# Optimization experiments

Hardware: AMD Instinct MI355X
Metric: run time of the kernel (lower is better)

Reference implementation:

```python
import jax, jax.numpy as jnp
import numpy as np

B, S, D = 2, 2048, 2048
H, G = 32, 8            # n_head, n_kv_groups
DH = D // H             # 64
HG = H // G             # heads per group = 4


def setup_inputs() -> dict:
    key = jax.random.key(0)
    ks = jax.random.split(key, 7)
    kv_dim = G * DH
    return {
        "q": jax.random.normal(ks[0], (B, S, D), jnp.float32),
        "k": jax.random.normal(ks[1], (B, S, D), jnp.float32),
        "v": jax.random.normal(ks[2], (B, S, D), jnp.float32),
        "mask": jnp.tril(jnp.ones((S, S), jnp.bool_)),  # causal
        "w_q": jax.random.normal(ks[3], (D, D), jnp.float32) * 0.02,
        "w_k": jax.random.normal(ks[4], (kv_dim, D), jnp.float32) * 0.02,
        "w_v": jax.random.normal(ks[5], (kv_dim, D), jnp.float32) * 0.02,
        "w_out": jax.random.normal(ks[6], (D, D), jnp.float32) * 0.02,
    }


def reference(q, k, v, mask, w_q, w_k, w_v, w_out):
    scale = 1.0 / np.sqrt(DH).astype(np.float32)
    # projections (F.linear: x @ W.T)
    qp = (q @ w_q.T).reshape(B, S, G, HG, DH)   # [b s g h d]
    kp = (k @ w_k.T).reshape(B, S, G, DH)       # [b t g d]
    vp = (v @ w_v.T).reshape(B, S, G, DH)
    # grouped attention scores [b g h s t]
    scores = jnp.einsum('bsghd,btgd->bghst', qp, kp) * scale
    scores = jnp.where(mask[None, None, None], scores, jnp.float32(-jnp.inf))
    attn = jax.nn.softmax(scores, axis=-1)
    out = jnp.einsum('bghst,btgd->bsghd', attn, vp).reshape(B, S, D)
    return out @ w_out.T
```

## Files before the change

### kernel.cpp

```cpp
#include <hip/hip_runtime.h>
#include <hip/hip_bf16.h>
#include <stdint.h>

#define B_SZ 2
#define S_LEN 2048
#define D_MODEL 2048
#define NH 32
#define NG 8
#define HGRP 4
#define DHEAD 64
#define KV_DIM 512
#define M_TOK 4096
#define KVB 64
#define QBLK 256

typedef __attribute__((ext_vector_type(8))) short bf16x8;
typedef __attribute__((ext_vector_type(4))) float f32x4;
typedef __attribute__((ext_vector_type(16))) float f32x16;

__device__ inline unsigned short f2bf(float x) {
    uint32_t u = __builtin_bit_cast(uint32_t, x);
    uint32_t r = (u + 0x7fffu + ((u >> 16) & 1u)) >> 16;
    return (unsigned short)r;
}

__device__ inline uint32_t cvtpk(float lo, float hi) {
    uint32_t r;
    asm("v_cvt_pk_bf16_f32 %0, %1, %2" : "=v"(r) : "v"(lo), "v"(hi));
    return r;
}

__device__ inline void plswap(uint32_t& a, uint32_t& b) {
    asm volatile("v_permlane32_swap_b32 %0, %1" : "+v"(a), "+v"(b));
}

__device__ inline float bf2f(unsigned short u) {
    uint32_t x = ((uint32_t)u) << 16;
    return __builtin_bit_cast(float, x);
}

__device__ inline void async_copy16(const void* g, void* l) {
    __builtin_amdgcn_global_load_lds(
        (const __attribute__((address_space(1))) void*)g,
        (__attribute__((address_space(3))) void*)l,
        16, 0, 0);
}

__device__ inline void gbar() {
    asm volatile("" ::: "memory");
    __builtin_amdgcn_s_barrier();
    asm volatile("" ::: "memory");
}
__device__ inline void lgkm0() {
    asm volatile("s_waitcnt lgkmcnt(0)" ::: "memory");
    __builtin_amdgcn_sched_barrier(0);
}

__device__ inline float vmax16(const f32x16& v) {
    float a0 = fmaxf(v[0], v[1]), a1 = fmaxf(v[2], v[3]);
    float a2 = fmaxf(v[4], v[5]), a3 = fmaxf(v[6], v[7]);
    float a4 = fmaxf(v[8], v[9]), a5 = fmaxf(v[10], v[11]);
    float a6 = fmaxf(v[12], v[13]), a7 = fmaxf(v[14], v[15]);
    float b0 = fmaxf(a0, a1), b1 = fmaxf(a2, a3);
    float b2 = fmaxf(a4, a5), b3 = fmaxf(a6, a7);
    return fmaxf(fmaxf(b0, b1), fmaxf(b2, b3));
}
__device__ inline float vsum16(const f32x16& v) {
    float a0 = v[0] + v[1], a1 = v[2] + v[3], a2 = v[4] + v[5], a3 = v[6] + v[7];
    float a4 = v[8] + v[9], a5 = v[10] + v[11], a6 = v[12] + v[13], a7 = v[14] + v[15];
    float b0 = a0 + a1, b1 = a2 + a3, b2 = a4 + a5, b3 = a6 + a7;
    return (b0 + b1) + (b2 + b3);
}

__global__ __launch_bounds__(256) void cvt_w(const float* __restrict__ wq,
                                             const float* __restrict__ wk,
                                             const float* __restrict__ wv,
                                             const float* __restrict__ wo,
                                             unsigned short* __restrict__ wqb,
                                             unsigned short* __restrict__ wkvb,
                                             unsigned short* __restrict__ wob) {
    const int i = blockIdx.x * 256 + threadIdx.x;
    const float* src; unsigned short* dst; int j;
    if (i < 524288)      { src = wq; dst = wqb; j = i; }
    else if (i < 655360) { src = wk; dst = wkvb; j = i - 524288; }
    else if (i < 786432) { src = wv; dst = wkvb + (size_t)KV_DIM * D_MODEL; j = i - 655360; }
    else                 { src = wo; dst = wob; j = i - 786432; }
    const float4* p = reinterpret_cast<const float4*>(src) + (size_t)j * 2;
    float4 a = p[0], b = p[1];
    union { unsigned short u[8]; uint4 v4; } r;
    r.u[0] = f2bf(a.x); r.u[1] = f2bf(a.y); r.u[2] = f2bf(a.z); r.u[3] = f2bf(a.w);
    r.u[4] = f2bf(b.x); r.u[5] = f2bf(b.y); r.u[6] = f2bf(b.z); r.u[7] = f2bf(b.w);
    reinterpret_cast<uint4*>(dst)[j] = r.v4;
}

#define SCALE_Q 0.1803368867f
#define GK 2048

__global__ __launch_bounds__(512, 2) void gemm8p(const float* __restrict__ Aqf,
                                                 const float* __restrict__ Akf,
                                                 const float* __restrict__ Avf,
                                                 const unsigned short* __restrict__ Bq,
                                                 const unsigned short* __restrict__ Bkv,
                                                 unsigned short* __restrict__ out_q,
                                                 unsigned short* __restrict__ out_k,
                                                 unsigned short* __restrict__ out_v) {
    __shared__ __align__(16) char lds[131072];

    const int tid = threadIdx.x;
    const int lane = tid & 63;
    const int w = tid >> 6;
    const int wm = w >> 2, wn = w & 3;
    const int l15 = lane & 15, l4 = lane >> 4;

    int bid = blockIdx.x;
    bid = (bid & 7) * 24 + (bid >> 3);
    const int mb = bid & 15, nb = bid >> 4;
    const int m0 = mb * 256;

    const float* Af;
    const unsigned short* Bp;
    int mode = 0, n0q = 0;
    if (nb < 8) {
        Af = Aqf; Bp = Bq + (size_t)(nb * 256) * GK; mode = 0; n0q = nb * 256;
    } else if (nb < 10) {
        Af = Akf; Bp = Bkv + (size_t)((nb - 8) * 256) * GK; mode = 1; n0q = (nb - 8) * 256;
    } else {
        Af = Avf; Bp = Bkv + (size_t)((nb - 10) * 256 + 512) * GK; mode = 2; n0q = (nb - 10) * 256;
    }

    const int srow = tid >> 3;
    const int gcol = (((tid & 7) * 16) ^ ((srow & 7) << 4)) >> 1;
    char* const myl = lds + tid * 16;

    float4 av[8];
    auto issueA = [&](int tile) {
#pragma unroll
        for (int h = 0; h < 2; ++h)
#pragma unroll
            for (int r2 = 0; r2 < 2; ++r2) {
                const float* s = Af + (size_t)(m0 + h * 128 + srow + r2 * 64) * GK + tile * 64 + gcol;
                av[(h * 2 + r2) * 2 + 0] = *reinterpret_cast<const float4*>(s);
                av[(h * 2 + r2) * 2 + 1] = *reinterpret_cast<const float4*>(s + 4);
            }
    };
    auto writeA = [&](int tile) {
#pragma unroll
        for (int h = 0; h < 2; ++h)
#pragma unroll
            for (int r2 = 0; r2 < 2; ++r2) {
                const float4 x = av[(h * 2 + r2) * 2 + 0];
                const float4 y = av[(h * 2 + r2) * 2 + 1];
                uint4 o;
                o.x = cvtpk(x.x, x.y); o.y = cvtpk(x.z, x.w);
                o.z = cvtpk(y.x, y.y); o.w = cvtpk(y.z, y.w);
                *reinterpret_cast<uint4*>(myl + (tile & 1) * 32768 + h * 16384 + r2 * 8192) = o;
            }
    };
    auto stageB = [&](int tile, int half) {
        char* dst = myl + 65536 + (tile & 1) * 32768 + half * 16384;
        const unsigned short* src = Bp + (size_t)(half * 128 + srow) * GK + tile * 64 + gcol;
        async_copy16(src, dst);
        async_copy16(src + (size_t)64 * GK, dst + 8192);
    };

    bf16x8 af[4][2], bf[4][2];
    auto loadA = [&](int buf, int mhalf) {
        const char* base = lds + buf * 32768;
#pragma unroll
        for (int mi = 0; mi < 4; ++mi) {
            const int r = wm * 128 + mhalf * 64 + mi * 16 + l15;
#pragma unroll
            for (int ks = 0; ks < 2; ++ks)
                af[mi][ks] = *reinterpret_cast<const bf16x8*>(
                    base + r * 128 + ((ks * 64 + l4 * 16) ^ ((r & 7) << 4)));
        }
    };
    auto loadB = [&](int buf, int nhalf) {
        const char* base = lds + 65536 + buf * 32768;
#pragma unroll
        for (int ni2 = 0; ni2 < 2; ++ni2) {
            const int ni = nhalf * 2 + ni2;
            const int r = wn * 64 + ni * 16 + l15;
#pragma unroll
            for (int ks = 0; ks < 2; ++ks)
                bf[ni][ks] = *reinterpret_cast<const bf16x8*>(
                    base + r * 128 + ((ks * 64 + l4 * 16) ^ ((r & 7) << 4)));
        }
    };

    f32x4 acc[8][4] = {};
    auto mfma16 = [&](int mq, int nq) {
        __builtin_amdgcn_s_setprio(1);
#pragma unroll
        for (int mi = 0; mi < 4; ++mi)
#pragma unroll
            for (int ni2 = 0; ni2 < 2; ++ni2)
#pragma unroll
                for (int ks = 0; ks < 2; ++ks)
                    acc[mq * 4 + mi][nq * 2 + ni2] = __builtin_amdgcn_mfma_f32_16x16x32_bf16(
                        af[mi][ks], bf[nq * 2 + ni2][ks], acc[mq * 4 + mi][nq * 2 + ni2], 0, 0, 0);
        __builtin_amdgcn_s_setprio(0);
    };

    issueA(0);
    stageB(0, 0); stageB(0, 1); stageB(1, 0); stageB(1, 1);
    writeA(0);
    asm volatile("s_waitcnt vmcnt(4) lgkmcnt(0)" ::: "memory");
    gbar();

    for (int i = 0; i < 16; ++i) {
        const int u = 2 * i;
        const bool nl = (i < 15);
        loadA(0, 0); loadB(0, 0); issueA(u + 1);
        gbar(); lgkm0(); mfma16(0, 0); gbar();
        loadB(0, 1);
        gbar(); lgkm0(); mfma16(0, 1); gbar();
        loadA(0, 1); if (nl) stageB(u + 2, 0);
        gbar(); lgkm0(); mfma16(1, 0); gbar();
        if (nl) stageB(u + 2, 1);
        gbar(); mfma16(1, 1);
        if (nl) asm volatile("s_waitcnt vmcnt(4)" ::: "memory");
        else    asm volatile("s_waitcnt vmcnt(0)" ::: "memory");
        writeA(u + 1);
        asm volatile("s_waitcnt lgkmcnt(0)" ::: "memory");
        gbar();
        loadA(1, 0); loadB(1, 0); if (nl) issueA(u + 2);
        gbar(); lgkm0(); mfma16(0, 0); gbar();
        loadB(1, 1);
        gbar(); lgkm0(); mfma16(0, 1); gbar();
        loadA(1, 1); if (nl) stageB(u + 3, 0);
        gbar(); lgkm0(); mfma16(1, 0); gbar();
        if (nl) stageB(u + 3, 1);
        gbar(); mfma16(1, 1);
        if (nl) {
            asm volatile("s_waitcnt vmcnt(4)" ::: "memory");
            writeA(u + 2);
        }
        asm volatile("s_waitcnt lgkmcnt(0)" ::: "memory");
        gbar();
    }

    if (mode == 0) {
#pragma unroll
        for (int mi = 0; mi < 8; ++mi) {
            const int row = m0 + wm * 128 + mi * 16 + l4 * 4;
#pragma unroll
            for (int ni = 0; ni < 4; ++ni) {
                const int col = n0q + wn * 64 + ni * 16 + l15;
#pragma unroll
                for (int r = 0; r < 4; ++r)
                    out_q[(size_t)(row + r) * D_MODEL + col] = f2bf(acc[mi][ni][r] * SCALE_Q);
            }
        }
    } else if (mode == 1) {
#pragma unroll
        for (int mi = 0; mi < 8; ++mi) {
            const int row = m0 + wm * 128 + mi * 16 + l4 * 4;
#pragma unroll
            for (int ni = 0; ni < 4; ++ni) {
                const int col = n0q + wn * 64 + ni * 16 + l15;
#pragma unroll
                for (int r = 0; r < 4; ++r)
                    out_k[(size_t)(row + r) * KV_DIM + col] = f2bf(acc[mi][ni][r]);
            }
        }
    } else {
        const int bb = m0 >> 11;
#pragma unroll
        for (int mi = 0; mi < 8; ++mi) {
            const int tok = (m0 & 2047) + wm * 128 + mi * 16 + l4 * 4;
#pragma unroll
            for (int ni = 0; ni < 4; ++ni) {
                const int c = n0q + wn * 64 + ni * 16 + l15;
                const int g = c >> 6, dh = c & 63;
                uint2 pk;
                pk.x = cvtpk(acc[mi][ni][0], acc[mi][ni][1]);
                pk.y = cvtpk(acc[mi][ni][2], acc[mi][ni][3]);
                *reinterpret_cast<uint2*>(out_v + (size_t)((bb * NG + g) * DHEAD + dh) * S_LEN + tok) = pk;
            }
        }
    }
}

__global__ __launch_bounds__(512, 1) void gemm8o(const unsigned short* __restrict__ A,
                                                 const unsigned short* __restrict__ B,
                                                 float* __restrict__ C) {
    __shared__ __align__(16) char lds[98304];

    const int tid = threadIdx.x;
    const int lane = tid & 63;
    const int w = tid >> 6;
    const int wm = w >> 1, wn = w & 1;
    const int l15 = lane & 15, l4 = lane >> 4;

    int bid = blockIdx.x;
    bid = (bid & 7) * 32 + (bid >> 3);
    const int mb = bid & 15, nb = bid >> 4;
    const int m0 = mb * 256, n0 = nb * 128;
    const unsigned short* Bp = B + (size_t)n0 * GK;

    const int srow = tid >> 3;
    const int gcol = (((tid & 7) * 16) ^ ((srow & 7) << 4)) >> 1;

    auto stageA = [&](int tile, int half) {
        char* dst = lds + (tile & 1) * 32768 + half * 16384 + tid * 16;
        const unsigned short* src = A + (size_t)(m0 + half * 128 + srow) * GK + tile * 64 + gcol;
        async_copy16(src, dst);
        async_copy16(src + (size_t)64 * GK, dst + 8192);
    };
    auto stageB = [&](int tile, int half) {
        char* dst = lds + 65536 + (tile & 1) * 16384 + half * 8192 + tid * 16;
        const unsigned short* src = Bp + (size_t)(half * 64 + srow) * GK + tile * 64 + gcol;
        async_copy16(src, dst);
    };

    bf16x8 af[2][2], bf[4][2];
    auto loadA2 = [&](int buf, int mhalf) {
        const char* base = lds + buf * 32768;
#pragma unroll
        for (int mi = 0; mi < 2; ++mi) {
            const int r = wm * 64 + mhalf * 32 + mi * 16 + l15;
#pragma unroll
            for (int ks = 0; ks < 2; ++ks)
                af[mi][ks] = *reinterpret_cast<const bf16x8*>(
                    base + r * 128 + ((ks * 64 + l4 * 16) ^ ((r & 7) << 4)));
        }
    };
    auto loadB2 = [&](int buf, int nhalf) {
        const char* base = lds + 65536 + buf * 16384;
#pragma unroll
        for (int ni2 = 0; ni2 < 2; ++ni2) {
            const int ni = nhalf * 2 + ni2;
            const int r = wn * 64 + ni * 16 + l15;
#pragma unroll
            for (int ks = 0; ks < 2; ++ks)
                bf[ni][ks] = *reinterpret_cast<const bf16x8*>(
                    base + r * 128 + ((ks * 64 + l4 * 16) ^ ((r & 7) << 4)));
        }
    };

    f32x4 acc[4][4] = {};
    auto mfma8 = [&](int mq, int nq) {
        __builtin_amdgcn_s_setprio(1);
#pragma unroll
        for (int mi = 0; mi < 2; ++mi)
#pragma unroll
            for (int ni2 = 0; ni2 < 2; ++ni2)
#pragma unroll
                for (int ks = 0; ks < 2; ++ks)
                    acc[mq * 2 + mi][nq * 2 + ni2] = __builtin_amdgcn_mfma_f32_16x16x32_bf16(
                        af[mi][ks], bf[nq * 2 + ni2][ks], acc[mq * 2 + mi][nq * 2 + ni2], 0, 0, 0);
        __builtin_amdgcn_s_setprio(0);
    };

    stageA(0, 0); stageA(0, 1); stageB(0, 0); stageB(0, 1); stageB(1, 0); stageB(1, 1);
    asm volatile("s_waitcnt vmcnt(2)" ::: "memory");
    gbar();

    for (int i = 0; i < 16; ++i) {
        const int u = 2 * i;
        const bool nl = (i < 15);
        loadA2(0, 0); loadB2(0, 0); stageA(u + 1, 0);
        gbar(); lgkm0(); mfma8(0, 0); gbar();
        loadB2(0, 1); stageA(u + 1, 1);
        gbar(); lgkm0(); mfma8(0, 1); gbar();
        loadA2(0, 1); if (nl) stageB(u + 2, 0);
        gbar(); lgkm0(); mfma8(1, 0); gbar();
        if (nl) stageB(u + 2, 1);
        gbar(); mfma8(1, 1);
        if (nl) asm volatile("s_waitcnt vmcnt(2)" ::: "memory");
        else    asm volatile("s_waitcnt vmcnt(0)" ::: "memory");
        gbar();
        loadA2(1, 0); loadB2(1, 0); if (nl) stageA(u + 2, 0);
        gbar(); lgkm0(); mfma8(0, 0); gbar();
        loadB2(1, 1); if (nl) stageA(u + 2, 1);
        gbar(); lgkm0(); mfma8(0, 1); gbar();
        loadA2(1, 1); if (nl) stageB(u + 3, 0);
        gbar(); lgkm0(); mfma8(1, 0); gbar();
        if (nl) stageB(u + 3, 1);
        gbar(); mfma8(1, 1);
        if (nl) asm volatile("s_waitcnt vmcnt(2)" ::: "memory");
        gbar();
    }

#pragma unroll
    for (int mi = 0; mi < 4; ++mi) {
        const int row = m0 + wm * 64 + mi * 16 + l4 * 4;
#pragma unroll
        for (int ni = 0; ni < 4; ++ni) {
            const int col = n0 + wn * 64 + ni * 16 + l15;
#pragma unroll
            for (int r = 0; r < 4; ++r)
                C[(size_t)(row + r) * D_MODEL + col] = acc[mi][ni][r];
        }
    }
}

__constant__ unsigned char sl_qi[16] = {7,7,7,6,6,6,5,5,5,4,4,3,3,2,1,0};
__constant__ unsigned char sl_j0[16] = {0,11,22,0,10,19,0,8,16,0,10,0,8,0,0,0};
__constant__ unsigned char sl_j1[16] = {11,22,32,10,19,28,8,16,24,10,20,8,16,12,8,4};
__constant__ unsigned char sl_pt[16] = {0,1,2,0,1,2,0,1,2,0,1,0,1,0,0,0};
__constant__ unsigned char pb_base[5] = {0,2,4,7,10};

__global__ __launch_bounds__(512, 4) void attn6_kernel(const unsigned short* __restrict__ qp,
                                                       const unsigned short* __restrict__ kp,
                                                       const unsigned short* __restrict__ vpT,
                                                       unsigned short* __restrict__ attn_out,
                                                       unsigned short* __restrict__ partO,
                                                       float* __restrict__ ml) {
    __shared__ __align__(16) unsigned short Ks[2][KVB * 64];
    __shared__ __align__(16) unsigned short Vs[2][KVB * 64];

    const int tid = threadIdx.x;
    const int lane = tid & 63;
    const int w = tid >> 6;
    const int l31 = lane & 31, hi = lane >> 5;
    const int sr = tid >> 3, sc = tid & 7;
    const int sgcol = (((sc * 16) ^ ((sr & 7) << 4)) >> 1);
    char* const kdst0 = (char*)Ks[0] + tid * 16;
    char* const kdst1 = (char*)Ks[1] + tid * 16;
    char* const vdst0 = (char*)Vs[0] + tid * 16;
    char* const vdst1 = (char*)Vs[1] + tid * 16;

    const int item = blockIdx.x;
    const int slot = item >> 6;
    const int bh = item & 63;
    const int qi = sl_qi[slot];
    const int j0 = sl_j0[slot];
    const int j1 = sl_j1[slot];
    const int part = sl_pt[slot];
    const bool merged = (qi >= 3);
    const int b = bh >> 5, head = bh & 31, g = head >> 2;
    const int s0 = qi * QBLK;
    const int m = s0 + w * 32 + l31;
    const int mmin = s0 + w * 32;
    const int mmaxw = mmin + 31;

    bf16x8 qf[4];
    {
        const unsigned short* qrow = qp + (size_t)(b * S_LEN + m) * D_MODEL + head * DHEAD + hi * 8;
#pragma unroll
        for (int k = 0; k < 4; ++k)
            qf[k] = *reinterpret_cast<const bf16x8*>(qrow + k * 16);
    }

    const unsigned short* kbase = kp + (size_t)(b * S_LEN + sr) * KV_DIM + g * DHEAD + sgcol;
    const unsigned short* vbase = vpT + (size_t)((b * NG + g) * DHEAD + sr) * S_LEN + sgcol;

    float mrun = -1e30f, lrun = 0.f;
    f32x16 o0 = {}, o1 = {};

    async_copy16(kbase + (size_t)j0 * KVB * KV_DIM, kdst0);
    async_copy16(vbase + j0 * KVB, vdst0);
    asm volatile("s_waitcnt vmcnt(0)" ::: "memory");
    gbar();

    for (int j = j0; j < j1; ++j) {
        const int cur = (j - j0) & 1;
        const int t0 = j * KVB;
        if (j + 1 < j1) {
            async_copy16(kbase + (size_t)(j + 1) * KVB * KV_DIM, cur ? kdst0 : kdst1);
            async_copy16(vbase + (j + 1) * KVB, cur ? vdst0 : vdst1);
        }

        const bool tt0 = (t0 <= mmaxw);
        const bool tt1 = (t0 + 32 <= mmaxw);
        if (tt0) {
            const char* Kb = (const char*)Ks[cur];
            const char* Vb = (const char*)Vs[cur];
            const int rswz0 = (l31 & 7) << 4;

            f32x16 s0v = {}, s1v = {};
#pragma unroll
            for (int k = 0; k < 4; ++k) {
                const int coff = k * 32 + hi * 16;
                const bf16x8 kf0 = *reinterpret_cast<const bf16x8*>(
                    Kb + l31 * 128 + (coff ^ rswz0));
                s0v = __builtin_amdgcn_mfma_f32_32x32x16_bf16(kf0, qf[k], s0v, 0, 0, 0);
                if (tt1) {
                    const bf16x8 kf1 = *reinterpret_cast<const bf16x8*>(
                        Kb + (32 + l31) * 128 + (coff ^ rswz0));
                    s1v = __builtin_amdgcn_mfma_f32_32x32x16_bf16(kf1, qf[k], s1v, 0, 0, 0);
                }
            }

            const bool msk = (t0 + KVB - 1) > mmin;
            if (msk) {
#pragma unroll
                for (int r = 0; r < 16; ++r) {
                    const int tloc = (r & 3) + 8 * (r >> 2) + 4 * hi;
                    if (t0 + tloc > m) s0v[r] = -1e30f;
                }
                if (tt1) {
#pragma unroll
                    for (int r = 0; r < 16; ++r) {
                        const int tloc = 32 + (r & 3) + 8 * (r >> 2) + 4 * hi;
                        if (t0 + tloc > m) s1v[r] = -1e30f;
                    }
                }
            }
            float rmax = vmax16(s0v);
            if (tt1) rmax = fmaxf(rmax, vmax16(s1v));
            rmax = fmaxf(rmax, __shfl_xor(rmax, 32, 64));
            if (!__all(rmax <= mrun + 8.0f)) {
                const float mnew = fmaxf(mrun, rmax);
                const float corr = __builtin_amdgcn_exp2f(mrun - mnew);
                lrun *= corr;
#pragma unroll
                for (int r = 0; r < 16; ++r) { o0[r] *= corr; o1[r] *= corr; }
                mrun = mnew;
            }
#pragma unroll
            for (int r = 0; r < 16; ++r)
                s0v[r] = __builtin_amdgcn_exp2f(s0v[r] - mrun);
            if (tt1) {
#pragma unroll
                for (int r = 0; r < 16; ++r)
                    s1v[r] = __builtin_amdgcn_exp2f(s1v[r] - mrun);
            }
            float rs = vsum16(s0v);
            if (tt1) rs += vsum16(s1v);
            rs += __shfl_xor(rs, 32, 64);
            lrun += rs;

#pragma unroll
            for (int c = 0; c < 4; ++c) {
                if (c >= 2 && !tt1) break;
                const f32x16& sv = (c >> 1) ? s1v : s0v;
                const int h8 = (c & 1) * 8;
                uint32_t a0 = cvtpk(sv[h8 + 0], sv[h8 + 1]);
                uint32_t a1 = cvtpk(sv[h8 + 2], sv[h8 + 3]);
                uint32_t b0 = cvtpk(sv[h8 + 4], sv[h8 + 5]);
                uint32_t b1 = cvtpk(sv[h8 + 6], sv[h8 + 7]);
                plswap(a0, b0); plswap(a1, b1);
                union { uint32_t w4[4]; bf16x8 v; } pf;
                pf.w4[0] = a0; pf.w4[1] = a1; pf.w4[2] = b0; pf.w4[3] = b1;
                const int coff = c * 32 + hi * 16;
                const bf16x8 vf0 = *reinterpret_cast<const bf16x8*>(
                    Vb + l31 * 128 + (coff ^ rswz0));
                o0 = __builtin_amdgcn_mfma_f32_32x32x16_bf16(vf0, pf.v, o0, 0, 0, 0);
                const bf16x8 vf1 = *reinterpret_cast<const bf16x8*>(
                    Vb + (32 + l31) * 128 + (coff ^ rswz0));
                o1 = __builtin_amdgcn_mfma_f32_32x32x16_bf16(vf1, pf.v, o1, 0, 0, 0);
            }
        }
        asm volatile("s_waitcnt vmcnt(0)" ::: "memory");
        gbar();
    }

    if (merged) {
        const int pb = bh * 13 + pb_base[qi - 3] + part;
        const int mrow = w * 32 + l31;
        if (hi == 0) {
            ml[pb * 512 + mrow] = mrun;
            ml[pb * 512 + 256 + mrow] = lrun;
        }
        unsigned short* dst = partO + (size_t)pb * 16384 + mrow * 64 + hi * 4;
#pragma unroll
        for (int qd = 0; qd < 4; ++qd) {
            uint2 pk0, pk1;
            pk0.x = cvtpk(o0[4 * qd + 0], o0[4 * qd + 1]);
            pk0.y = cvtpk(o0[4 * qd + 2], o0[4 * qd + 3]);
            pk1.x = cvtpk(o1[4 * qd + 0], o1[4 * qd + 1]);
            pk1.y = cvtpk(o1[4 * qd + 2], o1[4 * qd + 3]);
            *reinterpret_cast<uint2*>(dst + 8 * qd) = pk0;
            *reinterpret_cast<uint2*>(dst + 32 + 8 * qd) = pk1;
        }
    } else {
        const float inv = 1.0f / lrun;
        unsigned short* dst = attn_out + (size_t)(b * S_LEN + m) * D_MODEL + head * DHEAD + hi * 4;
#pragma unroll
        for (int qd = 0; qd < 4; ++qd) {
            uint2 pk0, pk1;
            pk0.x = cvtpk(o0[4 * qd + 0] * inv, o0[4 * qd + 1] * inv);
            pk0.y = cvtpk(o0[4 * qd + 2] * inv, o0[4 * qd + 3] * inv);
            pk1.x = cvtpk(o1[4 * qd + 0] * inv, o1[4 * qd + 1] * inv);
            pk1.y = cvtpk(o1[4 * qd + 2] * inv, o1[4 * qd + 3] * inv);
            *reinterpret_cast<uint2*>(dst + 8 * qd) = pk0;
            *reinterpret_cast<uint2*>(dst + 32 + 8 * qd) = pk1;
        }
    }
}

__global__ __launch_bounds__(512) void merge4_kernel(const unsigned short* __restrict__ partO,
                                                     const float* __restrict__ ml,
                                                     unsigned short* __restrict__ attn_out) {
    const int blk = blockIdx.x;
    const int bh = blk / 5;
    const int qi = 3 + (blk - bh * 5);
    const int np = (qi >= 5) ? 3 : 2;
    const int pb = bh * 13 + pb_base[qi - 3];
    const int b = bh >> 5, head = bh & 31;
    const int s0 = qi * QBLK;
    const int tid = threadIdx.x;
    const int row = tid >> 1, dh0 = (tid & 1) * 32;

    float m0 = ml[(pb + 0) * 512 + row], l0 = ml[(pb + 0) * 512 + 256 + row];
    float m1 = ml[(pb + 1) * 512 + row], l1 = ml[(pb + 1) * 512 + 256 + row];
    float m2 = -1e30f, l2 = 0.f;
    if (np == 3) { m2 = ml[(pb + 2) * 512 + row]; l2 = ml[(pb + 2) * 512 + 256 + row]; }
    const float M = fmaxf(fmaxf(m0, m1), m2);
    float w0 = __builtin_amdgcn_exp2f(m0 - M);
    float w1 = __builtin_amdgcn_exp2f(m1 - M);
    float w2 = (np == 3) ? __builtin_amdgcn_exp2f(m2 - M) : 0.f;
    const float inv = 1.0f / (l0 * w0 + l1 * w1 + l2 * w2);
    w0 *= inv; w1 *= inv; w2 *= inv;

    const uint4* p0 = reinterpret_cast<const uint4*>(partO + (size_t)(pb + 0) * 16384 + row * 64 + dh0);
    const uint4* p1 = reinterpret_cast<const uint4*>(partO + (size_t)(pb + 1) * 16384 + row * 64 + dh0);
    const uint4* p2 = reinterpret_cast<const uint4*>(partO + (size_t)(pb + 2) * 16384 + row * 64 + dh0);
    unsigned short* dst = attn_out + (size_t)(b * S_LEN + s0 + row) * D_MODEL + head * DHEAD + dh0;
#pragma unroll
    for (int c = 0; c < 4; ++c) {
        union { unsigned short u[8]; uint4 v; } ua, ub, uc, uo;
        ua.v = p0[c]; ub.v = p1[c];
        if (np == 3) uc.v = p2[c];
#pragma unroll
        for (int e = 0; e < 8; e += 2) {
            float x0 = bf2f(ua.u[e]) * w0 + bf2f(ub.u[e]) * w1;
            float x1 = bf2f(ua.u[e + 1]) * w0 + bf2f(ub.u[e + 1]) * w1;
            if (np == 3) {
                x0 += bf2f(uc.u[e]) * w2;
                x1 += bf2f(uc.u[e + 1]) * w2;
            }
            reinterpret_cast<uint32_t*>(uo.u)[e >> 1] = cvtpk(x0, x1);
        }
        reinterpret_cast<uint4*>(dst)[c] = uo.v;
    }
}

extern "C" void kernel_launch(void* const* d_in, const int* in_sizes, int n_in,
                              void* d_out, int out_size, void* d_ws, size_t ws_size,
                              hipStream_t stream) {
    const float* q     = (const float*)d_in[0];
    const float* k     = (const float*)d_in[1];
    const float* v     = (const float*)d_in[2];
    const float* w_q   = (const float*)d_in[4];
    const float* w_k   = (const float*)d_in[5];
    const float* w_v   = (const float*)d_in[6];
    const float* w_out = (const float*)d_in[7];

    char* ws = (char*)d_ws;
    size_t off = 0;
    auto alloc = [&](size_t n) { char* p = ws + off; off += (n + 255) & ~(size_t)255; return p; };
    unsigned short* scr1 = (unsigned short*)alloc((size_t)M_TOK * D_MODEL * 2);
    unsigned short* scr2 = (unsigned short*)alloc((size_t)M_TOK * D_MODEL * 2);
    unsigned short* scr3 = (unsigned short*)alloc((size_t)M_TOK * D_MODEL * 2);
    unsigned short* wqb  = (unsigned short*)alloc((size_t)D_MODEL * D_MODEL * 2);
    unsigned short* wkvb = (unsigned short*)alloc((size_t)2 * KV_DIM * D_MODEL * 2);
    unsigned short* wob  = (unsigned short*)alloc((size_t)D_MODEL * D_MODEL * 2);
    unsigned short* qpb  = (unsigned short*)alloc((size_t)M_TOK * D_MODEL * 2);
    unsigned short* kpb  = (unsigned short*)alloc((size_t)M_TOK * KV_DIM * 2);
    unsigned short* vtb  = (unsigned short*)alloc((size_t)M_TOK * KV_DIM * 2);
    unsigned short* aob  = (unsigned short*)alloc((size_t)M_TOK * D_MODEL * 2);
    (void)scr3;

    cvt_w<<<dim3(5120), dim3(256), 0, stream>>>(w_q, w_k, w_v, w_out, wqb, wkvb, wob);

    gemm8p<<<dim3(192), dim3(512), 0, stream>>>(q, k, v, wqb, wkvb, qpb, kpb, vtb);

    attn6_kernel<<<dim3(1024), dim3(512), 0, stream>>>(qpb, kpb, vtb, aob, scr2, (float*)scr1);
    merge4_kernel<<<dim3(320), dim3(512), 0, stream>>>(scr2, (float*)scr1, aob);

    gemm8o<<<dim3(256), dim3(512), 0, stream>>>(aob, wob, (float*)d_out);
}
```

Baseline: 223.4 us.

## Pre-convert activations to bf16 and use 256x128 async-copy GEMM for projections

Converts q, k and v to bf16 in a separate conversion pass along with the weights, instead of loading fp32 activations and converting them inside the projection GEMM. The projection GEMM now reuses the bf16 async-copy pipeline from the output GEMM, with 256x128 tiles and 384 blocks instead of 256x256 tiles and 192 blocks. This removes register-staged fp32 loads and in-loop conversion, and gives more blocks to fill the CUs. In exchange it adds an extra full read and write pass over the activations, and it reuses the bf16 buffers as scratch for attention.

```diff
diff --git a/kernel.cpp b/kernel.cpp
--- a/kernel.cpp
+++ b/kernel.cpp
@@ -72,19 +72,28 @@
     return (b0 + b1) + (b2 + b3);
 }
 
-__global__ __launch_bounds__(256) void cvt_w(const float* __restrict__ wq,
-                                             const float* __restrict__ wk,
-                                             const float* __restrict__ wv,
-                                             const float* __restrict__ wo,
-                                             unsigned short* __restrict__ wqb,
-                                             unsigned short* __restrict__ wkvb,
-                                             unsigned short* __restrict__ wob) {
+__global__ __launch_bounds__(256) void cvt_all(const float* __restrict__ q,
+                                               const float* __restrict__ k,
+                                               const float* __restrict__ v,
+                                               const float* __restrict__ wq,
+                                               const float* __restrict__ wk,
+                                               const float* __restrict__ wv,
+                                               const float* __restrict__ wo,
+                                               unsigned short* __restrict__ qb,
+                                               unsigned short* __restrict__ kb,
+                                               unsigned short* __restrict__ vb,
+                                               unsigned short* __restrict__ wqb,
+                                               unsigned short* __restrict__ wkvb,
+                                               unsigned short* __restrict__ wob) {
     const int i = blockIdx.x * 256 + threadIdx.x;
     const float* src; unsigned short* dst; int j;
-    if (i < 524288)      { src = wq; dst = wqb; j = i; }
-    else if (i < 655360) { src = wk; dst = wkvb; j = i - 524288; }
-    else if (i < 786432) { src = wv; dst = wkvb + (size_t)KV_DIM * D_MODEL; j = i - 655360; }
-    else                 { src = wo; dst = wob; j = i - 786432; }
+    if (i < 1048576)      { src = q;  dst = qb;  j = i; }
+    else if (i < 2097152) { src = k;  dst = kb;  j = i - 1048576; }
+    else if (i < 3145728) { src = v;  dst = vb;  j = i - 2097152; }
+    else if (i < 3670016) { src = wq; dst = wqb; j = i - 3145728; }
+    else if (i < 3801088) { src = wk; dst = wkvb; j = i - 3670016; }
+    else if (i < 3932160) { src = wv; dst = wkvb + (size_t)KV_DIM * D_MODEL; j = i - 3801088; }
+    else                  { src = wo; dst = wob; j = i - 3932160; }
     const float4* p = reinterpret_cast<const float4*>(src) + (size_t)j * 2;
     float4 a = p[0], b = p[1];
     union { unsigned short u[8]; uint4 v4; } r;
@@ -96,195 +105,14 @@
 #define SCALE_Q 0.1803368867f
 #define GK 2048
 
-__global__ __launch_bounds__(512, 2) void gemm8p(const float* __restrict__ Aqf,
-                                                 const float* __restrict__ Akf,
-                                                 const float* __restrict__ Avf,
+__global__ __launch_bounds__(512, 1) void gemm8p(const unsigned short* __restrict__ Aq,
+                                                 const unsigned short* __restrict__ Ak,
+                                                 const unsigned short* __restrict__ Av,
                                                  const unsigned short* __restrict__ Bq,
                                                  const unsigned short* __restrict__ Bkv,
                                                  unsigned short* __restrict__ out_q,
                                                  unsigned short* __restrict__ out_k,
                                                  unsigned short* __restrict__ out_v) {
-    __shared__ __align__(16) char lds[131072];
-
-    const int tid = threadIdx.x;
-    const int lane = tid & 63;
-    const int w = tid >> 6;
-    const int wm = w >> 2, wn = w & 3;
-    const int l15 = lane & 15, l4 = lane >> 4;
-
-    int bid = blockIdx.x;
-    bid = (bid & 7) * 24 + (bid >> 3);
-    const int mb = bid & 15, nb = bid >> 4;
-    const int m0 = mb * 256;
-
-    const float* Af;
-    const unsigned short* Bp;
-    int mode = 0, n0q = 0;
-    if (nb < 8) {
-        Af = Aqf; Bp = Bq + (size_t)(nb * 256) * GK; mode = 0; n0q = nb * 256;
-    } else if (nb < 10) {
-        Af = Akf; Bp = Bkv + (size_t)((nb - 8) * 256) * GK; mode = 1; n0q = (nb - 8) * 256;
-    } else {
-        Af = Avf; Bp = Bkv + (size_t)((nb - 10) * 256 + 512) * GK; mode = 2; n0q = (nb - 10) * 256;
-    }
-
-    const int srow = tid >> 3;
-    const int gcol = (((tid & 7) * 16) ^ ((srow & 7) << 4)) >> 1;
-    char* const myl = lds + tid * 16;
-
-    float4 av[8];
-    auto issueA = [&](int tile) {
-#pragma unroll
-        for (int h = 0; h < 2; ++h)
-#pragma unroll
-            for (int r2 = 0; r2 < 2; ++r2) {
-                const float* s = Af + (size_t)(m0 + h * 128 + srow + r2 * 64) * GK + tile * 64 + gcol;
-                av[(h * 2 + r2) * 2 + 0] = *reinterpret_cast<const float4*>(s);
-                av[(h * 2 + r2) * 2 + 1] = *reinterpret_cast<const float4*>(s + 4);
-            }
-    };
-    auto writeA = [&](int tile) {
-#pragma unroll
-        for (int h = 0; h < 2; ++h)
-#pragma unroll
-            for (int r2 = 0; r2 < 2; ++r2) {
-                const float4 x = av[(h * 2 + r2) * 2 + 0];
-                const float4 y = av[(h * 2 + r2) * 2 + 1];
-                uint4 o;
-                o.x = cvtpk(x.x, x.y); o.y = cvtpk(x.z, x.w);
-                o.z = cvtpk(y.x, y.y); o.w = cvtpk(y.z, y.w);
-                *reinterpret_cast<uint4*>(myl + (tile & 1) * 32768 + h * 16384 + r2 * 8192) = o;
-            }
-    };
-    auto stageB = [&](int tile, int half) {
-        char* dst = myl + 65536 + (tile & 1) * 32768 + half * 16384;
-        const unsigned short* src = Bp + (size_t)(half * 128 + srow) * GK + tile * 64 + gcol;
-        async_copy16(src, dst);
-        async_copy16(src + (size_t)64 * GK, dst + 8192);
-    };
-
-    bf16x8 af[4][2], bf[4][2];
-    auto loadA = [&](int buf, int mhalf) {
-        const char* base = lds + buf * 32768;
-#pragma unroll
-        for (int mi = 0; mi < 4; ++mi) {
-            const int r = wm * 128 + mhalf * 64 + mi * 16 + l15;
-#pragma unroll
-            for (int ks = 0; ks < 2; ++ks)
-                af[mi][ks] = *reinterpret_cast<const bf16x8*>(
-                    base + r * 128 + ((ks * 64 + l4 * 16) ^ ((r & 7) << 4)));
-        }
-    };
-    auto loadB = [&](int buf, int nhalf) {
-        const char* base = lds + 65536 + buf * 32768;
-#pragma unroll
-        for (int ni2 = 0; ni2 < 2; ++ni2) {
-            const int ni = nhalf * 2 + ni2;
-            const int r = wn * 64 + ni * 16 + l15;
-#pragma unroll
-            for (int ks = 0; ks < 2; ++ks)
-                bf[ni][ks] = *reinterpret_cast<const bf16x8*>(
-                    base + r * 128 + ((ks * 64 + l4 * 16) ^ ((r & 7) << 4)));
-        }
-    };
-
-    f32x4 acc[8][4] = {};
-    auto mfma16 = [&](int mq, int nq) {
-        __builtin_amdgcn_s_setprio(1);
-#pragma unroll
-        for (int mi = 0; mi < 4; ++mi)
-#pragma unroll
-            for (int ni2 = 0; ni2 < 2; ++ni2)
-#pragma unroll
-                for (int ks = 0; ks < 2; ++ks)
-                    acc[mq * 4 + mi][nq * 2 + ni2] = __builtin_amdgcn_mfma_f32_16x16x32_bf16(
-                        af[mi][ks], bf[nq * 2 + ni2][ks], acc[mq * 4 + mi][nq * 2 + ni2], 0, 0, 0);
-        __builtin_amdgcn_s_setprio(0);
-    };
-
-    issueA(0);
-    stageB(0, 0); stageB(0, 1); stageB(1, 0); stageB(1, 1);
-    writeA(0);
-    asm volatile("s_waitcnt vmcnt(4) lgkmcnt(0)" ::: "memory");
-    gbar();
-
-    for (int i = 0; i < 16; ++i) {
-        const int u = 2 * i;
-        const bool nl = (i < 15);
-        loadA(0, 0); loadB(0, 0); issueA(u + 1);
-        gbar(); lgkm0(); mfma16(0, 0); gbar();
-        loadB(0, 1);
-        gbar(); lgkm0(); mfma16(0, 1); gbar();
-        loadA(0, 1); if (nl) stageB(u + 2, 0);
-        gbar(); lgkm0(); mfma16(1, 0); gbar();
-        if (nl) stageB(u + 2, 1);
-        gbar(); mfma16(1, 1);
-        if (nl) asm volatile("s_waitcnt vmcnt(4)" ::: "memory");
-        else    asm volatile("s_waitcnt vmcnt(0)" ::: "memory");
-        writeA(u + 1);
-        asm volatile("s_waitcnt lgkmcnt(0)" ::: "memory");
-        gbar();
-        loadA(1, 0); loadB(1, 0); if (nl) issueA(u + 2);
-        gbar(); lgkm0(); mfma16(0, 0); gbar();
-        loadB(1, 1);
-        gbar(); lgkm0(); mfma16(0, 1); gbar();
-        loadA(1, 1); if (nl) stageB(u + 3, 0);
-        gbar(); lgkm0(); mfma16(1, 0); gbar();
-        if (nl) stageB(u + 3, 1);
-        gbar(); mfma16(1, 1);
-        if (nl) {
-            asm volatile("s_waitcnt vmcnt(4)" ::: "memory");
-            writeA(u + 2);
-        }
-        asm volatile("s_waitcnt lgkmcnt(0)" ::: "memory");
-        gbar();
-    }
-
-    if (mode == 0) {
-#pragma unroll
-        for (int mi = 0; mi < 8; ++mi) {
-            const int row = m0 + wm * 128 + mi * 16 + l4 * 4;
-#pragma unroll
-            for (int ni = 0; ni < 4; ++ni) {
-                const int col = n0q + wn * 64 + ni * 16 + l15;
-#pragma unroll
-                for (int r = 0; r < 4; ++r)
-                    out_q[(size_t)(row + r) * D_MODEL + col] = f2bf(acc[mi][ni][r] * SCALE_Q);
-            }
-        }
-    } else if (mode == 1) {
-#pragma unroll
-        for (int mi = 0; mi < 8; ++mi) {
-            const int row = m0 + wm * 128 + mi * 16 + l4 * 4;
-#pragma unroll
-            for (int ni = 0; ni < 4; ++ni) {
-                const int col = n0q + wn * 64 + ni * 16 + l15;
-#pragma unroll
-                for (int r = 0; r < 4; ++r)
-                    out_k[(size_t)(row + r) * KV_DIM + col] = f2bf(acc[mi][ni][r]);
-            }
-        }
-    } else {
-        const int bb = m0 >> 11;
-#pragma unroll
-        for (int mi = 0; mi < 8; ++mi) {
-            const int tok = (m0 & 2047) + wm * 128 + mi * 16 + l4 * 4;
-#pragma unroll
-            for (int ni = 0; ni < 4; ++ni) {
-                const int c = n0q + wn * 64 + ni * 16 + l15;
-                const int g = c >> 6, dh = c & 63;
-                uint2 pk;
-                pk.x = cvtpk(acc[mi][ni][0], acc[mi][ni][1]);
-                pk.y = cvtpk(acc[mi][ni][2], acc[mi][ni][3]);
-                *reinterpret_cast<uint2*>(out_v + (size_t)((bb * NG + g) * DHEAD + dh) * S_LEN + tok) = pk;
-            }
-        }
-    }
-}
-
-__global__ __launch_bounds__(512, 1) void gemm8o(const unsigned short* __restrict__ A,
-                                                 const unsigned short* __restrict__ B,
-                                                 float* __restrict__ C) {
     __shared__ __align__(16) char lds[98304];
 
     const int tid = threadIdx.x;
@@ -294,10 +122,20 @@
     const int l15 = lane & 15, l4 = lane >> 4;
 
     int bid = blockIdx.x;
-    bid = (bid & 7) * 32 + (bid >> 3);
+    bid = (bid & 7) * 48 + (bid >> 3);
     const int mb = bid & 15, nb = bid >> 4;
-    const int m0 = mb * 256, n0 = nb * 128;
-    const unsigned short* Bp = B + (size_t)n0 * GK;
+    const int m0 = mb * 256;
+
+    const unsigned short* A;
+    const unsigned short* Bp;
+    int mode, n0q;
+    if (nb < 16) {
+        A = Aq; Bp = Bq + (size_t)(nb * 128) * GK; mode = 0; n0q = nb * 128;
+    } else if (nb < 20) {
+        A = Ak; Bp = Bkv + (size_t)((nb - 16) * 128) * GK; mode = 1; n0q = (nb - 16) * 128;
+    } else {
+        A = Av; Bp = Bkv + (size_t)((nb - 20) * 128 + 512) * GK; mode = 2; n0q = (nb - 20) * 128;
+    }
 
     const int srow = tid >> 3;
     const int gcol = (((tid & 7) * 16) ^ ((srow & 7) << 4)) >> 1;
@@ -383,6 +221,149 @@
         gbar();
     }
 
+    if (mode == 0) {
+#pragma unroll
+        for (int mi = 0; mi < 4; ++mi) {
+            const int row = m0 + wm * 64 + mi * 16 + l4 * 4;
+#pragma unroll
+            for (int ni = 0; ni < 4; ++ni) {
+                const int col = n0q + wn * 64 + ni * 16 + l15;
+#pragma unroll
+                for (int r = 0; r < 4; ++r)
+                    out_q[(size_t)(row + r) * D_MODEL + col] = f2bf(acc[mi][ni][r] * SCALE_Q);
+            }
+        }
+    } else if (mode == 1) {
+#pragma unroll
+        for (int mi = 0; mi < 4; ++mi) {
+            const int row = m0 + wm * 64 + mi * 16 + l4 * 4;
+#pragma unroll
+            for (int ni = 0; ni < 4; ++ni) {
+                const int col = n0q + wn * 64 + ni * 16 + l15;
+#pragma unroll
+                for (int r = 0; r < 4; ++r)
+                    out_k[(size_t)(row + r) * KV_DIM + col] = f2bf(acc[mi][ni][r]);
+            }
+        }
+    } else {
+        const int bb = m0 >> 11;
+#pragma unroll
+        for (int mi = 0; mi < 4; ++mi) {
+            const int tok = (m0 & 2047) + wm * 64 + mi * 16 + l4 * 4;
+#pragma unroll
+            for (int ni = 0; ni < 4; ++ni) {
+                const int c = n0q + wn * 64 + ni * 16 + l15;
+                const int g = c >> 6, dh = c & 63;
+                uint2 pk;
+                pk.x = cvtpk(acc[mi][ni][0], acc[mi][ni][1]);
+                pk.y = cvtpk(acc[mi][ni][2], acc[mi][ni][3]);
+                *reinterpret_cast<uint2*>(out_v + (size_t)((bb * NG + g) * DHEAD + dh) * S_LEN + tok) = pk;
+            }
+        }
+    }
+}
+
+__global__ __launch_bounds__(512, 1) void gemm8o(const unsigned short* __restrict__ A,
+                                                 const unsigned short* __restrict__ B,
+                                                 float* __restrict__ C) {
+    __shared__ __align__(16) char lds[98304];
+
+    const int tid = threadIdx.x;
+    const int lane = tid & 63;
+    const int w = tid >> 6;
+    const int wm = w >> 1, wn = w & 1;
+    const int l15 = lane & 15, l4 = lane >> 4;
+
+    int bid = blockIdx.x;
+    bid = (bid & 7) * 32 + (bid >> 3);
+    const int mb = bid & 15, nb = bid >> 4;
+    const int m0 = mb * 256, n0 = nb * 128;
+    const unsigned short* Bp = B + (size_t)n0 * GK;
+
+    const int srow = tid >> 3;
+    const int gcol = (((tid & 7) * 16) ^ ((srow & 7) << 4)) >> 1;
+
+    auto stageA = [&](int tile, int half) {
+        char* dst = lds + (tile & 1) * 32768 + half * 16384 + tid * 16;
+        const unsigned short* src = A + (size_t)(m0 + half * 128 + srow) * GK + tile * 64 + gcol;
+        async_copy16(src, dst);
+        async_copy16(src + (size_t)64 * GK, dst + 8192);
+    };
+    auto stageB = [&](int tile, int half) {
+        char* dst = lds + 65536 + (tile & 1) * 16384 + half * 8192 + tid * 16;
+        const unsigned short* src = Bp + (size_t)(half * 64 + srow) * GK + tile * 64 + gcol;
+        async_copy16(src, dst);
+    };
+
+    bf16x8 af[2][2], bf[4][2];
+    auto loadA2 = [&](int buf, int mhalf) {
+        const char* base = lds + buf * 32768;
+#pragma unroll
+        for (int mi = 0; mi < 2; ++mi) {
+            const int r = wm * 64 + mhalf * 32 + mi * 16 + l15;
+#pragma unroll
+            for (int ks = 0; ks < 2; ++ks)
+                af[mi][ks] = *reinterpret_cast<const bf16x8*>(
+                    base + r * 128 + ((ks * 64 + l4 * 16) ^ ((r & 7) << 4)));
+        }
+    };
+    auto loadB2 = [&](int buf, int nhalf) {
+        const char* base = lds + 65536 + buf * 16384;
+#pragma unroll
+        for (int ni2 = 0; ni2 < 2; ++ni2) {
+            const int ni = nhalf * 2 + ni2;
+            const int r = wn * 64 + ni * 16 + l15;
+#pragma unroll
+            for (int ks = 0; ks < 2; ++ks)
+                bf[ni][ks] = *reinterpret_cast<const bf16x8*>(
+                    base + r * 128 + ((ks * 64 + l4 * 16) ^ ((r & 7) << 4)));
+        }
+    };
+
+    f32x4 acc[4][4] = {};
+    auto mfma8 = [&](int mq, int nq) {
+        __builtin_amdgcn_s_setprio(1);
+#pragma unroll
+        for (int mi = 0; mi < 2; ++mi)
+#pragma unroll
+            for (int ni2 = 0; ni2 < 2; ++ni2)
+#pragma unroll
+                for (int ks = 0; ks < 2; ++ks)
+                    acc[mq * 2 + mi][nq * 2 + ni2] = __builtin_amdgcn_mfma_f32_16x16x32_bf16(
+                        af[mi][ks], bf[nq * 2 + ni2][ks], acc[mq * 2 + mi][nq * 2 + ni2], 0, 0, 0);
+        __builtin_amdgcn_s_setprio(0);
+    };
+
+    stageA(0, 0); stageA(0, 1); stageB(0, 0); stageB(0, 1); stageB(1, 0); stageB(1, 1);
+    asm volatile("s_waitcnt vmcnt(2)" ::: "memory");
+    gbar();
+
+    for (int i = 0; i < 16; ++i) {
+        const int u = 2 * i;
+        const bool nl = (i < 15);
+        loadA2(0, 0); loadB2(0, 0); stageA(u + 1, 0);
+        gbar(); lgkm0(); mfma8(0, 0); gbar();
+        loadB2(0, 1); stageA(u + 1, 1);
+        gbar(); lgkm0(); mfma8(0, 1); gbar();
+        loadA2(0, 1); if (nl) stageB(u + 2, 0);
+        gbar(); lgkm0(); mfma8(1, 0); gbar();
+        if (nl) stageB(u + 2, 1);
+        gbar(); mfma8(1, 1);
+        if (nl) asm volatile("s_waitcnt vmcnt(2)" ::: "memory");
+        else    asm volatile("s_waitcnt vmcnt(0)" ::: "memory");
+        gbar();
+        loadA2(1, 0); loadB2(1, 0); if (nl) stageA(u + 2, 0);
+        gbar(); lgkm0(); mfma8(0, 0); gbar();
+        loadB2(1, 1); if (nl) stageA(u + 2, 1);
+        gbar(); lgkm0(); mfma8(0, 1); gbar();
+        loadA2(1, 1); if (nl) stageB(u + 3, 0);
+        gbar(); lgkm0(); mfma8(1, 0); gbar();
+        if (nl) stageB(u + 3, 1);
+        gbar(); mfma8(1, 1);
+        if (nl) asm volatile("s_waitcnt vmcnt(2)" ::: "memory");
+        gbar();
+    }
+
 #pragma unroll
     for (int mi = 0; mi < 4; ++mi) {
         const int row = m0 + wm * 64 + mi * 16 + l4 * 4;
@@ -643,9 +624,9 @@
     char* ws = (char*)d_ws;
     size_t off = 0;
     auto alloc = [&](size_t n) { char* p = ws + off; off += (n + 255) & ~(size_t)255; return p; };
-    unsigned short* scr1 = (unsigned short*)alloc((size_t)M_TOK * D_MODEL * 2);
-    unsigned short* scr2 = (unsigned short*)alloc((size_t)M_TOK * D_MODEL * 2);
-    unsigned short* scr3 = (unsigned short*)alloc((size_t)M_TOK * D_MODEL * 2);
+    unsigned short* qb   = (unsigned short*)alloc((size_t)M_TOK * D_MODEL * 2);
+    unsigned short* kb   = (unsigned short*)alloc((size_t)M_TOK * D_MODEL * 2);
+    unsigned short* vb   = (unsigned short*)alloc((size_t)M_TOK * D_MODEL * 2);
     unsigned short* wqb  = (unsigned short*)alloc((size_t)D_MODEL * D_MODEL * 2);
     unsigned short* wkvb = (unsigned short*)alloc((size_t)2 * KV_DIM * D_MODEL * 2);
     unsigned short* wob  = (unsigned short*)alloc((size_t)D_MODEL * D_MODEL * 2);
@@ -653,14 +634,14 @@
     unsigned short* kpb  = (unsigned short*)alloc((size_t)M_TOK * KV_DIM * 2);
     unsigned short* vtb  = (unsigned short*)alloc((size_t)M_TOK * KV_DIM * 2);
     unsigned short* aob  = (unsigned short*)alloc((size_t)M_TOK * D_MODEL * 2);
-    (void)scr3;
-
-    cvt_w<<<dim3(5120), dim3(256), 0, stream>>>(w_q, w_k, w_v, w_out, wqb, wkvb, wob);
-
-    gemm8p<<<dim3(192), dim3(512), 0, stream>>>(q, k, v, wqb, wkvb, qpb, kpb, vtb);
-
-    attn6_kernel<<<dim3(1024), dim3(512), 0, stream>>>(qpb, kpb, vtb, aob, scr2, (float*)scr1);
-    merge4_kernel<<<dim3(320), dim3(512), 0, stream>>>(scr2, (float*)scr1, aob);
+
+    cvt_all<<<dim3(17408), dim3(256), 0, stream>>>(q, k, v, w_q, w_k, w_v, w_out,
+                                                   qb, kb, vb, wqb, wkvb, wob);
+
+    gemm8p<<<dim3(384), dim3(512), 0, stream>>>(qb, kb, vb, wqb, wkvb, qpb, kpb, vtb);
+
+    attn6_kernel<<<dim3(1024), dim3(512), 0, stream>>>(qpb, kpb, vtb, aob, kb, (float*)qb);
+    merge4_kernel<<<dim3(320), dim3(512), 0, stream>>>(kb, (float*)qb, aob);
 
     gemm8o<<<dim3(256), dim3(512), 0, stream>>>(aob, wob, (float*)d_out);
 }
```

Result: faster. 213.4 us (-4.5%).
